# Optimization experiments

Hardware: AMD Instinct MI355X
Metric: run time of the kernel (lower is better)

The kernel has to match this reference:

```python
import jax, jax.numpy as jnp
import numpy as np

B, N, H, HEADS, PH, VD = 32, 256, 768, 12, 128, 16
DH = H // HEADS
VOCAB = 2 * VD + 3


def layer_norm(x, g, b, eps=1e-5):
    m = jnp.mean(x, axis=-1, keepdims=True)
    v = jnp.mean((x - m) ** 2, axis=-1, keepdims=True)
    return (x - m) * jax.lax.rsqrt(v + eps) * g + b


def setup_inputs() -> dict:
    key = jax.random.key(0)
    ks = jax.random.split(key, 12)
    # clamped relative-distance index pool, as in PathEmbeddingDistance
    t = np.arange(N)
    pool = t[None, :] - t[:, None]
    pool = np.clip(pool, -VD - 1, VD + 1) + VD + 1  # in [0, 2*VD+2]
    s = 0.02
    return {
        "nodes": jax.random.normal(ks[0], (B, N, H), jnp.float32),
        "bias": jnp.zeros((B, 1, 1, N), jnp.float32),
        "path_pool": jnp.asarray(pool, jnp.int32),
        "pos_table": jax.random.normal(ks[1], (VOCAB, PH), jnp.float32) * s,
        "Wq": jax.random.normal(ks[2], (H, H), jnp.float32) * s, "bq": jnp.zeros((H,), jnp.float32),
        "Wk": jax.random.normal(ks[3], (H, H), jnp.float32) * s, "bk": jnp.zeros((H,), jnp.float32),
        "Wv": jax.random.normal(ks[4], (H, H), jnp.float32) * s, "bv": jnp.zeros((H,), jnp.float32),
        "Wsk": jax.random.normal(ks[5], (PH, DH), jnp.float32) * s, "bsk": jnp.zeros((DH,), jnp.float32),
        "Wsv": jax.random.normal(ks[6], (PH, DH), jnp.float32) * s, "bsv": jnp.zeros((DH,), jnp.float32),
        "Wo": jax.random.normal(ks[7], (H, H), jnp.float32) * s, "bo": jnp.zeros((H,), jnp.float32),
        "g_path": jnp.ones((PH,), jnp.float32), "b_path": jnp.zeros((PH,), jnp.float32),
        "g_norm": jnp.ones((H,), jnp.float32), "b_norm": jnp.zeros((H,), jnp.float32),
    }


def reference(nodes, bias, path_pool, pos_table, Wq, bq, Wk, bk, Wv, bv,
              Wsk, bsk, Wsv, bsv, Wo, bo, g_path, b_path, g_norm, b_norm):
    # path embedding lookup (batch-independent: torch expand == broadcast)
    paths = pos_table[path_pool]                      # (N, N, PH)
    paths = layer_norm(paths, g_path, b_path)
    q = (nodes @ Wq + bq).reshape(B, N, HEADS, DH).transpose(0, 2, 1, 3)
    k = (nodes @ Wk + bk).reshape(B, N, HEADS, DH).transpose(0, 2, 1, 3)
    v = (nodes @ Wv + bv).reshape(B, N, HEADS, DH).transpose(0, 2, 1, 3)
    struct_k = paths @ Wsk + bsk                      # (N, N, DH)
    struct_v = paths @ Wsv + bsv                      # (N, N, DH)
    q = q * (DH ** -0.5)
    w = jnp.einsum("bhid,bhjd->bhij", q, k)
    struct_w = jnp.einsum("bhid,ijd->bhij", q, struct_k)
    w = jax.nn.softmax(w + struct_w + bias, axis=-1)  # (B, HEADS, N, N)
    out = jnp.einsum("bhij,bhjd->bhid", w, v) + jnp.einsum("bhij,ijd->bhid", w, struct_v)
    out = out.transpose(0, 2, 1, 3).reshape(B, N, H)  # combine heads
    out = jax.nn.relu(out @ Wo + bo)
    return layer_norm(nodes + out, g_norm, b_norm), w
```

## Files before the change

### kernel.cpp

```cpp
#include <hip/hip_runtime.h>
#include <hip/hip_bf16.h>

#define BB 32
#define NN 256
#define HH 768
#define NHEADS 12
#define DH 64
#define PHDIM 128
#define NVOCAB 35

typedef short bf16x8 __attribute__((ext_vector_type(8)));
typedef float f32x16 __attribute__((ext_vector_type(16)));
typedef unsigned u32x2 __attribute__((ext_vector_type(2)));

#define MFMA32 __builtin_amdgcn_mfma_f32_32x32x16_bf16

__device__ __forceinline__ unsigned short f2bf(float f) {
    unsigned u = __float_as_uint(f);
    unsigned r = (u + 0x7fffu + ((u >> 16) & 1u)) >> 16;
    return (unsigned short)r;
}

__device__ __forceinline__ unsigned pk2(float a, float b) {
    return (unsigned)f2bf(a) | ((unsigned)f2bf(b) << 16);
}

__device__ __forceinline__ bf16x8 pack8(const float f[8]) {
    bf16x8 r;
#pragma unroll
    for (int e = 0; e < 8; ++e) r[e] = (short)f2bf(f[e]);
    return r;
}

__global__ __launch_bounds__(256) void k_cast(const float* __restrict__ in,
                                              unsigned short* __restrict__ out) {
    int i = (blockIdx.x * 256 + threadIdx.x) * 4;
    float4 v = *reinterpret_cast<const float4*>(&in[i]);
    ushort4 o;
    o.x = f2bf(v.x); o.y = f2bf(v.y); o.z = f2bf(v.z); o.w = f2bf(v.w);
    *reinterpret_cast<ushort4*>(&out[i]) = o;
}

__global__ __launch_bounds__(256) void k_prep_w(
        const float* __restrict__ Wq, const float* __restrict__ Wk,
        const float* __restrict__ Wv, const float* __restrict__ Wo,
        unsigned short* __restrict__ Wt) {
    __shared__ unsigned short tile[64][72];
    int z = blockIdx.z;
    const float* W = (z == 0) ? Wq : (z == 1) ? Wk : (z == 2) ? Wv : Wo;
    unsigned short* out = Wt + (size_t)z * HH * HH;
    int k0 = blockIdx.x * 64, c0 = blockIdx.y * 64;
    int tid = threadIdx.x;
#pragma unroll
    for (int l = 0; l < 16; ++l) {
        int e = tid + l * 256;
        int r = e >> 6, c = e & 63;
        tile[c][r] = f2bf(W[(size_t)(k0 + r) * HH + c0 + c]);
    }
    __syncthreads();
#pragma unroll
    for (int l = 0; l < 2; ++l) {
        int e = tid + l * 256;
        int c = e >> 3, ch = e & 7;
        *reinterpret_cast<bf16x8*>(&out[(size_t)(c0 + c) * HH + k0 + ch * 8]) =
            *reinterpret_cast<const bf16x8*>(&tile[c][ch * 8]);
    }
}

__global__ void k_vocab(const float* __restrict__ pos_table,
                        const float* __restrict__ g_path, const float* __restrict__ b_path,
                        const float* __restrict__ Wsk, const float* __restrict__ bsk,
                        const float* __restrict__ Wsv, const float* __restrict__ bsv,
                        unsigned short* __restrict__ skv_bf, unsigned short* __restrict__ svv_t_bf) {
    int v = blockIdx.x;
    int t = threadIdx.x;
    if (v >= NVOCAB) {
        if (t < 64) skv_bf[v * 64 + t] = 0;
        else if (v < 48) svv_t_bf[(t - 64) * 48 + v] = 0;
        return;
    }
    __shared__ float x[PHDIM];
    __shared__ float red[PHDIM];
    float xv = pos_table[v * PHDIM + t];
    red[t] = xv;
    __syncthreads();
    for (int s = 64; s > 0; s >>= 1) { if (t < s) red[t] += red[t + s]; __syncthreads(); }
    float mean = red[0] / PHDIM;
    __syncthreads();
    float c = xv - mean;
    red[t] = c * c;
    __syncthreads();
    for (int s = 64; s > 0; s >>= 1) { if (t < s) red[t] += red[t + s]; __syncthreads(); }
    float var = red[0] / PHDIM;
    float ln = (xv - mean) * rsqrtf(var + 1e-5f) * g_path[t] + b_path[t];
    __syncthreads();
    x[t] = ln;
    __syncthreads();
    if (t < 64) {
        float acc = bsk[t];
        for (int p = 0; p < PHDIM; ++p) acc += x[p] * Wsk[p * DH + t];
        skv_bf[v * 64 + t] = f2bf(acc);
    } else {
        int d = t - 64;
        float acc = bsv[d];
        for (int p = 0; p < PHDIM; ++p) acc += x[p] * Wsv[p * DH + d];
        svv_t_bf[d * 48 + v] = f2bf(acc);
    }
}

__global__ __launch_bounds__(256) void k_qkv(
        const unsigned short* __restrict__ Abf, const unsigned short* __restrict__ Wt,
        const float* __restrict__ bq, const float* __restrict__ bk, const float* __restrict__ bv,
        unsigned short* __restrict__ q_bf, unsigned short* __restrict__ k_bf,
        unsigned short* __restrict__ v_bf_t) {
    __shared__ unsigned short Al[2][128 * 32];
    __shared__ unsigned short Bl[2][128 * 32];
    __shared__ unsigned short vstage[128][136];

    const int tid = threadIdx.x;
    const int w = tid >> 6, lane = tid & 63;
    const int il = lane & 31, hi = lane >> 5;
    const int wr = w >> 1, wc = w & 1;
    const int rowBase = blockIdx.x * 128;
    const int colBase = blockIdx.y * 128;
    const int sel = colBase / HH;
    const int jjBase0 = colBase - sel * HH;
    const float* bias = (sel == 0) ? bq : (sel == 1) ? bk : bv;

    f32x16 acc[2][2] = {};

    auto STAGE = [&](int buf, int k0) {
#pragma unroll
        for (int c = 0; c < 2; ++c) {
            int e = tid + c * 256;
            int row = e >> 2;
            int cb = (e & 3) << 4;
            int sc = cb ^ (((row >> 1) & 3) << 4);
            __builtin_amdgcn_global_load_lds(
                (const __attribute__((address_space(1))) unsigned int*)(Abf + (size_t)(rowBase + row) * HH + k0 + (sc >> 1)),
                (__attribute__((address_space(3))) unsigned int*)(&Al[buf][row * 32 + (cb >> 1)]), 16, 0, 0);
            __builtin_amdgcn_global_load_lds(
                (const __attribute__((address_space(1))) unsigned int*)(Wt + (size_t)(colBase + row) * HH + k0 + (sc >> 1)),
                (__attribute__((address_space(3))) unsigned int*)(&Bl[buf][row * 32 + (cb >> 1)]), 16, 0, 0);
        }
    };

    STAGE(0, 0);
    __syncthreads();
    for (int t = 0; t < 24; ++t) {
        int buf = t & 1;
        if (t < 23) STAGE(buf ^ 1, (t + 1) * 32);
#pragma unroll
        for (int ks = 0; ks < 2; ++ks) {
            bf16x8 af[2], bfr[2];
            int cb = (ks << 5) + (hi << 4);
#pragma unroll
            for (int t2 = 0; t2 < 2; ++t2) {
                int rrow = wr * 64 + t2 * 32 + il;
                af[t2] = *reinterpret_cast<const bf16x8*>(
                    &Al[buf][rrow * 32 + ((cb ^ (((rrow >> 1) & 3) << 4)) >> 1)]);
                int crow = wc * 64 + t2 * 32 + il;
                bfr[t2] = *reinterpret_cast<const bf16x8*>(
                    &Bl[buf][crow * 32 + ((cb ^ (((crow >> 1) & 3) << 4)) >> 1)]);
            }
            acc[0][0] = MFMA32(af[0], bfr[0], acc[0][0], 0, 0, 0);
            acc[0][1] = MFMA32(af[0], bfr[1], acc[0][1], 0, 0, 0);
            acc[1][0] = MFMA32(af[1], bfr[0], acc[1][0], 0, 0, 0);
            acc[1][1] = MFMA32(af[1], bfr[1], acc[1][1], 0, 0, 0);
        }
        __syncthreads();
    }

    if (sel < 2) {
        unsigned short* outp = (sel == 0) ? q_bf : k_bf;
        float scale = (sel == 0) ? 0.125f : 1.0f;
#pragma unroll
        for (int rt = 0; rt < 2; ++rt)
#pragma unroll
            for (int ct = 0; ct < 2; ++ct) {
                int jjB = jjBase0 + wc * 64 + ct * 32;
                int h = jjB >> 6, d = (jjB & 63) + il;
                float bias_v = bias[jjB + il];
#pragma unroll
                for (int r = 0; r < 16; ++r) {
                    int row = rowBase + wr * 64 + rt * 32 + ((r & 3) + 8 * (r >> 2) + 4 * hi);
                    int b = row >> 8, n = row & 255;
                    outp[((size_t)(b * NHEADS + h) * NN + n) * DH + d] =
                        f2bf((acc[rt][ct][r] + bias_v) * scale);
                }
            }
    } else {
#pragma unroll
        for (int rt = 0; rt < 2; ++rt)
#pragma unroll
            for (int ct = 0; ct < 2; ++ct) {
                int jjB = jjBase0 + wc * 64 + ct * 32;
                float bias_v = bias[jjB + il];
#pragma unroll
                for (int r = 0; r < 16; ++r) {
                    int rl = wr * 64 + rt * 32 + ((r & 3) + 8 * (r >> 2) + 4 * hi);
                    vstage[wc * 64 + ct * 32 + il][rl] = f2bf(acc[rt][ct][r] + bias_v);
                }
            }
        __syncthreads();
        int b = rowBase >> 8, n0 = rowBase & 255;
        int h0 = jjBase0 >> 6;
#pragma unroll
        for (int l = 0; l < 8; ++l) {
            int e = tid + l * 256;
            int cl = e >> 4;
            int nch = e & 15;
            size_t orow = (size_t)(b * NHEADS + h0 + (cl >> 6)) * DH + (cl & 63);
            *reinterpret_cast<bf16x8*>(&v_bf_t[orow * NN + n0 + nch * 8]) =
                *reinterpret_cast<const bf16x8*>(&vstage[cl][nch * 8]);
        }
    }
}

__global__ __launch_bounds__(256, 4) void k_attn(
        const unsigned short* __restrict__ q_bf, const unsigned short* __restrict__ k_bf,
        const unsigned short* __restrict__ v_bf_t,
        const unsigned short* __restrict__ skv_bf, const unsigned short* __restrict__ svv_t_bf,
        const float* __restrict__ bias,
        float* __restrict__ wout, unsigned short* __restrict__ attn_out) {
    __shared__ __align__(16) float qs_s[32][36];
    __shared__ __align__(16) float wsum[32][48];
    __shared__ __align__(16) float oex[3][32][68];
    __shared__ float msum[4][32][2];
    __shared__ float bias_s[NN];

    const int bx0 = blockIdx.x;
    const int bx = (bx0 & 7) * 384 + (bx0 >> 3);
    const int bh = bx >> 3, rowblk = bx & 7;
    const int b = bh / NHEADS, h = bh - b * NHEADS;
    const int tid = threadIdx.x;
    const int w = tid >> 6, lane = tid & 63;
    const int il = lane & 31, hi = lane >> 5;
    const int i0 = rowblk * 32;
    const int ig = i0 + il;
    const int jb = w * 64;

    bias_s[tid] = bias[b * NN + tid];
#pragma unroll
    for (int z = 0; z < 6; ++z) ((float*)wsum)[tid + z * 256] = 0.f;

    bf16x8 qf[4];
#pragma unroll
    for (int kt = 0; kt < 4; ++kt)
        qf[kt] = *reinterpret_cast<const bf16x8*>(
            &q_bf[((size_t)(bh * NN + ig)) * 64 + kt * 16 + 8 * hi]);

    if (w == 0) {
        f32x16 qa0 = {}, qa1 = {};
#pragma unroll
        for (int kt = 0; kt < 4; ++kt) {
            bf16x8 s0 = *reinterpret_cast<const bf16x8*>(&skv_bf[(size_t)il * 64 + kt * 16 + 8 * hi]);
            bf16x8 s1 = *reinterpret_cast<const bf16x8*>(&skv_bf[(size_t)(32 + il) * 64 + kt * 16 + 8 * hi]);
            qa0 = MFMA32(qf[kt], s0, qa0, 0, 0, 0);
            qa1 = MFMA32(qf[kt], s1, qa1, 0, 0, 0);
        }
#pragma unroll
        for (int r = 0; r < 16; ++r) {
            int ir = (r & 3) + 8 * (r >> 2) + 4 * hi;
            qs_s[ir][il] = qa0[r];
            if (il < 3) qs_s[ir][32 + il] = qa1[r];
        }
    }

    f32x16 S[2] = {};
#pragma unroll
    for (int jt = 0; jt < 2; ++jt) {
#pragma unroll
        for (int kt = 0; kt < 4; ++kt) {
            bf16x8 kf = *reinterpret_cast<const bf16x8*>(
                &k_bf[((size_t)(bh * NN + jb + jt * 32 + il)) * 64 + kt * 16 + 8 * hi]);
            S[jt] = MFMA32(kf, qf[kt], S[jt], 0, 0, 0);
        }
    }

    __syncthreads();

    {
        float qlo = qs_s[il][0], qhi = qs_s[il][34];
#pragma unroll
        for (int jt = 0; jt < 2; ++jt) {
#pragma unroll
            for (int rg = 0; rg < 4; ++rg) {
                int j0 = jb + jt * 32 + rg * 8 + 4 * hi;
                float4 bv4 = *reinterpret_cast<const float4*>(&bias_s[j0]);
                float bvf[4] = {bv4.x, bv4.y, bv4.z, bv4.w};
#pragma unroll
                for (int e = 0; e < 4; ++e) {
                    int dd = j0 + e - ig;
                    float sw = (dd < -16) ? qlo : (dd > 16) ? qhi : qs_s[il][dd + 17];
                    S[jt][rg * 4 + e] += bvf[e] + sw;
                }
            }
        }
    }

    float m = -3.4e38f;
#pragma unroll
    for (int jt = 0; jt < 2; ++jt)
#pragma unroll
        for (int r = 0; r < 16; ++r) m = fmaxf(m, S[jt][r]);
    m = fmaxf(m, __shfl_xor(m, 32));
    float sum = 0.f;
#pragma unroll
    for (int jt = 0; jt < 2; ++jt)
#pragma unroll
        for (int r = 0; r < 16; ++r) { float p = __expf(S[jt][r] - m); S[jt][r] = p; sum += p; }
    sum += __shfl_xor(sum, 32);
    if (hi == 0) { msum[w][il][0] = m; msum[w][il][1] = sum; }
    __syncthreads();

    {
        float m0 = msum[0][il][0], m1 = msum[1][il][0];
        float m2 = msum[2][il][0], m3 = msum[3][il][0];
        float M = fmaxf(fmaxf(m0, m1), fmaxf(m2, m3));
        float sumT = msum[0][il][1] * __expf(m0 - M) + msum[1][il][1] * __expf(m1 - M) +
                     msum[2][il][1] * __expf(m2 - M) + msum[3][il][1] * __expf(m3 - M);
        float scale = __expf(m - M) / sumT;
#pragma unroll
        for (int jt = 0; jt < 2; ++jt)
#pragma unroll
            for (int r = 0; r < 16; ++r) S[jt][r] *= scale;
    }

#pragma unroll
    for (int jt = 0; jt < 2; ++jt) {
#pragma unroll
        for (int rg = 0; rg < 4; ++rg) {
            float4 val;
            val.x = S[jt][rg * 4 + 0];
            val.y = S[jt][rg * 4 + 1];
            val.z = S[jt][rg * 4 + 2];
            val.w = S[jt][rg * 4 + 3];
            *reinterpret_cast<float4*>(
                &wout[((size_t)(bh * NN + ig)) * NN + jb + jt * 32 + rg * 8 + 4 * hi]) = val;
        }
    }

    {
        float elo = 0.f, ehi = 0.f;
#pragma unroll
        for (int jt = 0; jt < 2; ++jt)
#pragma unroll
            for (int r = 0; r < 16; ++r) {
                int j = jb + jt * 32 + (r & 3) + 8 * (r >> 2) + 4 * hi;
                int dd = j - ig;
                float p = S[jt][r];
                if (dd < -16) elo += p;
                else if (dd > 16) ehi += p;
                else wsum[il][dd + 17] = p;
            }
        if (elo != 0.f) atomicAdd(&wsum[il][0], elo);
        if (ehi != 0.f) atomicAdd(&wsum[il][34], ehi);
    }

    const unsigned short* vrow0 = &v_bf_t[((size_t)bh * 64 + il) * NN];
    const unsigned short* vrow1 = &v_bf_t[((size_t)bh * 64 + 32 + il) * NN];
    f32x16 O0 = {}, O1 = {};
#pragma unroll
    for (int jt = 0; jt < 2; ++jt) {
#pragma unroll
        for (int ks = 0; ks < 2; ++ks) {
            unsigned w0 = pk2(S[jt][8 * ks + 0], S[jt][8 * ks + 1]);
            unsigned w1 = pk2(S[jt][8 * ks + 2], S[jt][8 * ks + 3]);
            unsigned w2 = pk2(S[jt][8 * ks + 4], S[jt][8 * ks + 5]);
            unsigned w3 = pk2(S[jt][8 * ks + 6], S[jt][8 * ks + 7]);
            unsigned s0 = hi ? w0 : w2, s1 = hi ? w1 : w3;
            unsigned y0 = (unsigned)__shfl_xor((int)s0, 32);
            unsigned y1 = (unsigned)__shfl_xor((int)s1, 32);
            union { bf16x8 v; unsigned u[4]; } Bf;
            Bf.u[0] = hi ? y0 : w0;
            Bf.u[1] = hi ? y1 : w1;
            Bf.u[2] = hi ? w2 : y0;
            Bf.u[3] = hi ? w3 : y1;
            bf16x8 va0 = *reinterpret_cast<const bf16x8*>(&vrow0[jb + jt * 32 + ks * 16 + 8 * hi]);
            bf16x8 va1 = *reinterpret_cast<const bf16x8*>(&vrow1[jb + jt * 32 + ks * 16 + 8 * hi]);
            O0 = MFMA32(va0, Bf.v, O0, 0, 0, 0);
            O1 = MFMA32(va1, Bf.v, O1, 0, 0, 0);
        }
    }

    if (w != 0) {
#pragma unroll
        for (int qq = 0; qq < 4; ++qq) {
            int d0 = 8 * qq + 4 * hi;
            *reinterpret_cast<float4*>(&oex[w - 1][il][d0]) =
                float4{O0[4 * qq + 0], O0[4 * qq + 1], O0[4 * qq + 2], O0[4 * qq + 3]};
            *reinterpret_cast<float4*>(&oex[w - 1][il][32 + d0]) =
                float4{O1[4 * qq + 0], O1[4 * qq + 1], O1[4 * qq + 2], O1[4 * qq + 3]};
        }
    }
    __syncthreads();

    if (w == 0) {
#pragma unroll
        for (int s = 0; s < 3; ++s) {
#pragma unroll
            for (int qq = 0; qq < 4; ++qq) {
                int d0 = 8 * qq + 4 * hi;
                float4 p0 = *reinterpret_cast<const float4*>(&oex[s][il][d0]);
                float4 p1 = *reinterpret_cast<const float4*>(&oex[s][il][32 + d0]);
                O0[4 * qq + 0] += p0.x; O0[4 * qq + 1] += p0.y;
                O0[4 * qq + 2] += p0.z; O0[4 * qq + 3] += p0.w;
                O1[4 * qq + 0] += p1.x; O1[4 * qq + 1] += p1.y;
                O1[4 * qq + 2] += p1.z; O1[4 * qq + 3] += p1.w;
            }
        }

#pragma unroll
        for (int kt = 0; kt < 3; ++kt) {
            float4 a0 = *reinterpret_cast<const float4*>(&wsum[il][kt * 16 + 8 * hi]);
            float4 a1 = *reinterpret_cast<const float4*>(&wsum[il][kt * 16 + 8 * hi + 4]);
            float af[8] = {a0.x, a0.y, a0.z, a0.w, a1.x, a1.y, a1.z, a1.w};
            bf16x8 Bf = pack8(af);
            bf16x8 sa0 = *reinterpret_cast<const bf16x8*>(&svv_t_bf[(size_t)il * 48 + kt * 16 + 8 * hi]);
            bf16x8 sa1 = *reinterpret_cast<const bf16x8*>(&svv_t_bf[(size_t)(32 + il) * 48 + kt * 16 + 8 * hi]);
            O0 = MFMA32(sa0, Bf, O0, 0, 0, 0);
            O1 = MFMA32(sa1, Bf, O1, 0, 0, 0);
        }

#pragma unroll
        for (int qq = 0; qq < 4; ++qq) {
            int d0 = 8 * qq + 4 * hi;
            u32x2 o0, o1;
            o0[0] = pk2(O0[4 * qq + 0], O0[4 * qq + 1]);
            o0[1] = pk2(O0[4 * qq + 2], O0[4 * qq + 3]);
            o1[0] = pk2(O1[4 * qq + 0], O1[4 * qq + 1]);
            o1[1] = pk2(O1[4 * qq + 2], O1[4 * qq + 3]);
            size_t base = ((size_t)(b * NN + i0 + il)) * HH + h * 64;
            *reinterpret_cast<u32x2*>(&attn_out[base + d0]) = o0;
            *reinterpret_cast<u32x2*>(&attn_out[base + 32 + d0]) = o1;
        }
    }
}

__global__ __launch_bounds__(256) void k_ogemm(
        const unsigned short* __restrict__ Abf, const unsigned short* __restrict__ Bt,
        const float* __restrict__ bo, unsigned short* __restrict__ Cout) {
    __shared__ unsigned short Al[2][128 * 32];
    __shared__ unsigned short Bl[2][128 * 32];

    const int tid = threadIdx.x;
    const int w = tid >> 6, lane = tid & 63;
    const int il = lane & 31, hi = lane >> 5;
    const int wr = w >> 1, wc = w & 1;
    const int rowBase = blockIdx.x * 128;
    const int colBase = blockIdx.y * 128;

    f32x16 acc[2][2] = {};

    auto STAGE = [&](int buf, int k0) {
#pragma unroll
        for (int c = 0; c < 2; ++c) {
            int e = tid + c * 256;
            int row = e >> 2;
            int cb = (e & 3) << 4;
            int sc = cb ^ (((row >> 1) & 3) << 4);
            __builtin_amdgcn_global_load_lds(
                (const __attribute__((address_space(1))) unsigned int*)(Abf + (size_t)(rowBase + row) * HH + k0 + (sc >> 1)),
                (__attribute__((address_space(3))) unsigned int*)(&Al[buf][row * 32 + (cb >> 1)]), 16, 0, 0);
            __builtin_amdgcn_global_load_lds(
                (const __attribute__((address_space(1))) unsigned int*)(Bt + (size_t)(colBase + row) * HH + k0 + (sc >> 1)),
                (__attribute__((address_space(3))) unsigned int*)(&Bl[buf][row * 32 + (cb >> 1)]), 16, 0, 0);
        }
    };

    STAGE(0, 0);
    __syncthreads();
    for (int t = 0; t < 24; ++t) {
        int buf = t & 1;
        if (t < 23) STAGE(buf ^ 1, (t + 1) * 32);
#pragma unroll
        for (int ks = 0; ks < 2; ++ks) {
            bf16x8 af[2], bfr[2];
            int cb = (ks << 5) + (hi << 4);
#pragma unroll
            for (int t2 = 0; t2 < 2; ++t2) {
                int rrow = wr * 64 + t2 * 32 + il;
                af[t2] = *reinterpret_cast<const bf16x8*>(
                    &Al[buf][rrow * 32 + ((cb ^ (((rrow >> 1) & 3) << 4)) >> 1)]);
                int crow = wc * 64 + t2 * 32 + il;
                bfr[t2] = *reinterpret_cast<const bf16x8*>(
                    &Bl[buf][crow * 32 + ((cb ^ (((crow >> 1) & 3) << 4)) >> 1)]);
            }
            acc[0][0] = MFMA32(af[0], bfr[0], acc[0][0], 0, 0, 0);
            acc[0][1] = MFMA32(af[0], bfr[1], acc[0][1], 0, 0, 0);
            acc[1][0] = MFMA32(af[1], bfr[0], acc[1][0], 0, 0, 0);
            acc[1][1] = MFMA32(af[1], bfr[1], acc[1][1], 0, 0, 0);
        }
        __syncthreads();
    }

#pragma unroll
    for (int rt = 0; rt < 2; ++rt)
#pragma unroll
        for (int ct = 0; ct < 2; ++ct) {
            int col = colBase + wc * 64 + ct * 32 + il;
            float bias_v = bo[col];
#pragma unroll
            for (int r = 0; r < 16; ++r) {
                int row = rowBase + wr * 64 + rt * 32 + ((r & 3) + 8 * (r >> 2) + 4 * hi);
                Cout[(size_t)row * HH + col] = f2bf(fmaxf(acc[rt][ct][r] + bias_v, 0.f));
            }
        }
}

__global__ __launch_bounds__(256) void k_ln(
        const float* __restrict__ nodes, const unsigned short* __restrict__ proj,
        const float* __restrict__ g, const float* __restrict__ bta,
        float* __restrict__ out) {
    __shared__ float red[2][4];
    int row = blockIdx.x;
    int tid = threadIdx.x;
    int w = tid >> 6, lane = tid & 63;
    float x[3];
    float s = 0.f, s2 = 0.f;
#pragma unroll
    for (int l = 0; l < 3; ++l) {
        int c = tid + l * 256;
        float pv = __uint_as_float(((unsigned)proj[(size_t)row * HH + c]) << 16);
        x[l] = nodes[(size_t)row * HH + c] + pv;
        s += x[l];
        s2 += x[l] * x[l];
    }
#pragma unroll
    for (int off = 32; off > 0; off >>= 1) {
        s += __shfl_xor(s, off);
        s2 += __shfl_xor(s2, off);
    }
    if (lane == 0) { red[0][w] = s; red[1][w] = s2; }
    __syncthreads();
    float ts = red[0][0] + red[0][1] + red[0][2] + red[0][3];
    float ts2 = red[1][0] + red[1][1] + red[1][2] + red[1][3];
    float mean = ts / HH;
    float var = ts2 / HH - mean * mean;
    float inv = rsqrtf(fmaxf(var, 0.f) + 1e-5f);
#pragma unroll
    for (int l = 0; l < 3; ++l) {
        int c = tid + l * 256;
        out[(size_t)row * HH + c] = (x[l] - mean) * inv * g[c] + bta[c];
    }
}

extern "C" void kernel_launch(void* const* d_in, const int* in_sizes, int n_in,
                              void* d_out, int out_size, void* d_ws, size_t ws_size,
                              hipStream_t stream) {
    const float* nodes     = (const float*)d_in[0];
    const float* bias      = (const float*)d_in[1];
    const float* pos_table = (const float*)d_in[3];
    const float* Wq = (const float*)d_in[4];  const float* bq = (const float*)d_in[5];
    const float* Wk = (const float*)d_in[6];  const float* bk = (const float*)d_in[7];
    const float* Wv = (const float*)d_in[8];  const float* bv = (const float*)d_in[9];
    const float* Wsk = (const float*)d_in[10]; const float* bsk = (const float*)d_in[11];
    const float* Wsv = (const float*)d_in[12]; const float* bsv = (const float*)d_in[13];
    const float* Wo = (const float*)d_in[14]; const float* bo = (const float*)d_in[15];
    const float* g_path = (const float*)d_in[16]; const float* b_path = (const float*)d_in[17];
    const float* g_norm = (const float*)d_in[18]; const float* b_norm = (const float*)d_in[19];

    float* out0 = (float*)d_out;
    float* wout = out0 + (size_t)BB * NN * HH;

    const size_t per = (size_t)BB * NN * HH;
    char* p = (char*)d_ws;
    unsigned short* q_bf    = (unsigned short*)p; p += per * 2;
    unsigned short* k_bf    = (unsigned short*)p; p += per * 2;
    unsigned short* v_bf_t  = (unsigned short*)p; p += per * 2;
    unsigned short* skv_bf  = (unsigned short*)p; p += 64 * 64 * 2;
    unsigned short* svv_t   = (unsigned short*)p; p += 64 * 48 * 2;
    unsigned short* nodes_bf= (unsigned short*)p; p += per * 2;
    unsigned short* Wt      = (unsigned short*)p; p += (size_t)4 * HH * HH * 2;
    unsigned short* attn_bf = (unsigned short*)p; p += per * 2;
    unsigned short* proj_bf = v_bf_t;

    k_cast<<<per / 4 / 256, 256, 0, stream>>>(nodes, nodes_bf);

    dim3 gw(12, 12, 4);
    k_prep_w<<<gw, 256, 0, stream>>>(Wq, Wk, Wv, Wo, Wt);

    k_vocab<<<64, 128, 0, stream>>>(pos_table, g_path, b_path, Wsk, bsk, Wsv, bsv, skv_bf, svv_t);

    dim3 g2(64, 18);
    k_qkv<<<g2, 256, 0, stream>>>(nodes_bf, Wt, bq, bk, bv, q_bf, k_bf, v_bf_t);

    k_attn<<<BB * NHEADS * 8, 256, 0, stream>>>(q_bf, k_bf, v_bf_t, skv_bf, svv_t, bias, wout, attn_bf);

    dim3 g4(64, 6);
    k_ogemm<<<g4, 256, 0, stream>>>(attn_bf, Wt + (size_t)3 * HH * HH, bo, proj_bf);

    k_ln<<<BB * NN, 256, 0, stream>>>(nodes, proj_bf, g_norm, b_norm, out0);
}
```

Measured before the change: 158.4 us.

## Store Q/K/V in MFMA fragment order and merge prep kernels into one launch

```diff
diff --git a/kernel.cpp b/kernel.cpp
--- a/kernel.cpp
+++ b/kernel.cpp
@@ -32,79 +32,86 @@
     return r;
 }
 
-__global__ __launch_bounds__(256) void k_cast(const float* __restrict__ in,
-                                              unsigned short* __restrict__ out) {
-    int i = (blockIdx.x * 256 + threadIdx.x) * 4;
-    float4 v = *reinterpret_cast<const float4*>(&in[i]);
-    ushort4 o;
-    o.x = f2bf(v.x); o.y = f2bf(v.y); o.z = f2bf(v.z); o.w = f2bf(v.w);
-    *reinterpret_cast<ushort4*>(&out[i]) = o;
-}
-
-__global__ __launch_bounds__(256) void k_prep_w(
+__global__ __launch_bounds__(256) void k_prep(
+        const float* __restrict__ nodes, unsigned short* __restrict__ nodes_bf,
         const float* __restrict__ Wq, const float* __restrict__ Wk,
         const float* __restrict__ Wv, const float* __restrict__ Wo,
-        unsigned short* __restrict__ Wt) {
-    __shared__ unsigned short tile[64][72];
-    int z = blockIdx.z;
-    const float* W = (z == 0) ? Wq : (z == 1) ? Wk : (z == 2) ? Wv : Wo;
-    unsigned short* out = Wt + (size_t)z * HH * HH;
-    int k0 = blockIdx.x * 64, c0 = blockIdx.y * 64;
-    int tid = threadIdx.x;
-#pragma unroll
-    for (int l = 0; l < 16; ++l) {
-        int e = tid + l * 256;
-        int r = e >> 6, c = e & 63;
-        tile[c][r] = f2bf(W[(size_t)(k0 + r) * HH + c0 + c]);
-    }
-    __syncthreads();
-#pragma unroll
-    for (int l = 0; l < 2; ++l) {
-        int e = tid + l * 256;
-        int c = e >> 3, ch = e & 7;
-        *reinterpret_cast<bf16x8*>(&out[(size_t)(c0 + c) * HH + k0 + ch * 8]) =
-            *reinterpret_cast<const bf16x8*>(&tile[c][ch * 8]);
-    }
-}
-
-__global__ void k_vocab(const float* __restrict__ pos_table,
-                        const float* __restrict__ g_path, const float* __restrict__ b_path,
-                        const float* __restrict__ Wsk, const float* __restrict__ bsk,
-                        const float* __restrict__ Wsv, const float* __restrict__ bsv,
-                        unsigned short* __restrict__ skv_bf, unsigned short* __restrict__ svv_t_bf) {
-    int v = blockIdx.x;
-    int t = threadIdx.x;
-    if (v >= NVOCAB) {
-        if (t < 64) skv_bf[v * 64 + t] = 0;
-        else if (v < 48) svv_t_bf[(t - 64) * 48 + v] = 0;
+        unsigned short* __restrict__ Wt,
+        const float* __restrict__ pos_table,
+        const float* __restrict__ g_path, const float* __restrict__ b_path,
+        const float* __restrict__ Wsk, const float* __restrict__ bsk,
+        const float* __restrict__ Wsv, const float* __restrict__ bsv,
+        unsigned short* __restrict__ skv_bf, unsigned short* __restrict__ svv_t_bf) {
+    const int blk = blockIdx.x;
+    const int tid = threadIdx.x;
+
+    if (blk < 6144) {
+        int i = (blk * 256 + tid) * 4;
+        float4 v = *reinterpret_cast<const float4*>(&nodes[i]);
+        ushort4 o;
+        o.x = f2bf(v.x); o.y = f2bf(v.y); o.z = f2bf(v.z); o.w = f2bf(v.w);
+        *reinterpret_cast<ushort4*>(&nodes_bf[i]) = o;
         return;
     }
-    __shared__ float x[PHDIM];
-    __shared__ float red[PHDIM];
-    float xv = pos_table[v * PHDIM + t];
-    red[t] = xv;
-    __syncthreads();
-    for (int s = 64; s > 0; s >>= 1) { if (t < s) red[t] += red[t + s]; __syncthreads(); }
-    float mean = red[0] / PHDIM;
-    __syncthreads();
-    float c = xv - mean;
-    red[t] = c * c;
-    __syncthreads();
-    for (int s = 64; s > 0; s >>= 1) { if (t < s) red[t] += red[t + s]; __syncthreads(); }
-    float var = red[0] / PHDIM;
-    float ln = (xv - mean) * rsqrtf(var + 1e-5f) * g_path[t] + b_path[t];
-    __syncthreads();
-    x[t] = ln;
-    __syncthreads();
-    if (t < 64) {
-        float acc = bsk[t];
-        for (int p = 0; p < PHDIM; ++p) acc += x[p] * Wsk[p * DH + t];
-        skv_bf[v * 64 + t] = f2bf(acc);
-    } else {
-        int d = t - 64;
-        float acc = bsv[d];
-        for (int p = 0; p < PHDIM; ++p) acc += x[p] * Wsv[p * DH + d];
-        svv_t_bf[d * 48 + v] = f2bf(acc);
+
+    if (blk < 6720) {
+        __shared__ unsigned short tile[64][72];
+        int wb = blk - 6144;
+        int z = wb / 144;
+        int rem = wb - z * 144;
+        int k0 = (rem / 12) * 64, c0 = (rem % 12) * 64;
+        const float* W = (z == 0) ? Wq : (z == 1) ? Wk : (z == 2) ? Wv : Wo;
+        unsigned short* out = Wt + (size_t)z * HH * HH;
+#pragma unroll
+        for (int l = 0; l < 16; ++l) {
+            int e = tid + l * 256;
+            int r = e >> 6, c = e & 63;
+            tile[c][r] = f2bf(W[(size_t)(k0 + r) * HH + c0 + c]);
+        }
+        __syncthreads();
+#pragma unroll
+        for (int l = 0; l < 2; ++l) {
+            int e = tid + l * 256;
+            int c = e >> 3, ch = e & 7;
+            *reinterpret_cast<bf16x8*>(&out[(size_t)(c0 + c) * HH + k0 + ch * 8]) =
+                *reinterpret_cast<const bf16x8*>(&tile[c][ch * 8]);
+        }
+        return;
+    }
+
+    {
+        int v = blk - 6720;
+        int t = tid;
+        if (v >= NVOCAB) {
+            if (t < 64) skv_bf[v * 64 + t] = 0;
+            else if (t < 128 && v < 48) svv_t_bf[(t - 64) * 48 + v] = 0;
+            return;
+        }
+        __shared__ float x[PHDIM];
+        __shared__ float red[PHDIM];
+        float xv = 0.f;
+        if (t < PHDIM) { xv = pos_table[v * PHDIM + t]; red[t] = xv; }
+        __syncthreads();
+        for (int s = 64; s > 0; s >>= 1) { if (t < s) red[t] += red[t + s]; __syncthreads(); }
+        float mean = red[0] / PHDIM;
+        __syncthreads();
+        if (t < PHDIM) { float c = xv - mean; red[t] = c * c; }
+        __syncthreads();
+        for (int s = 64; s > 0; s >>= 1) { if (t < s) red[t] += red[t + s]; __syncthreads(); }
+        float var = red[0] / PHDIM;
+        __syncthreads();
+        if (t < PHDIM) x[t] = (xv - mean) * rsqrtf(var + 1e-5f) * g_path[t] + b_path[t];
+        __syncthreads();
+        if (t < 64) {
+            float acc = bsk[t];
+            for (int p = 0; p < PHDIM; ++p) acc += x[p] * Wsk[p * DH + t];
+            skv_bf[v * 64 + t] = f2bf(acc);
+        } else if (t < 128) {
+            int d = t - 64;
+            float acc = bsv[d];
+            for (int p = 0; p < PHDIM; ++p) acc += x[p] * Wsv[p * DH + d];
+            svv_t_bf[d * 48 + v] = f2bf(acc);
+        }
     }
 }
 
@@ -179,14 +186,18 @@
 #pragma unroll
             for (int ct = 0; ct < 2; ++ct) {
                 int jjB = jjBase0 + wc * 64 + ct * 32;
-                int h = jjB >> 6, d = (jjB & 63) + il;
+                int h = jjB >> 6;
+                int d = ct * 32 + il;
+                int kt = d >> 4, hif = (d >> 3) & 1, e = d & 7;
                 float bias_v = bias[jjB + il];
 #pragma unroll
                 for (int r = 0; r < 16; ++r) {
                     int row = rowBase + wr * 64 + rt * 32 + ((r & 3) + 8 * (r >> 2) + 4 * hi);
                     int b = row >> 8, n = row & 255;
-                    outp[((size_t)(b * NHEADS + h) * NN + n) * DH + d] =
-                        f2bf((acc[rt][ct][r] + bias_v) * scale);
+                    int jr = n & 31, t32 = n >> 5;
+                    size_t off = ((((size_t)(b * NHEADS + h) * 8 + t32) * 4 + kt) * 64 +
+                                  (hif * 32 + jr)) * 8 + e;
+                    outp[off] = f2bf((acc[rt][ct][r] + bias_v) * scale);
                 }
             }
     } else {
@@ -207,12 +218,20 @@
         int h0 = jjBase0 >> 6;
 #pragma unroll
         for (int l = 0; l < 8; ++l) {
-            int e = tid + l * 256;
-            int cl = e >> 4;
-            int nch = e & 15;
-            size_t orow = (size_t)(b * NHEADS + h0 + (cl >> 6)) * DH + (cl & 63);
-            *reinterpret_cast<bf16x8*>(&v_bf_t[orow * NN + n0 + nch * 8]) =
-                *reinterpret_cast<const bf16x8*>(&vstage[cl][nch * 8]);
+            int idx = tid + l * 256;
+            int cl = idx >> 4;
+            int ch = idx & 15;
+            int tl0 = ch * 8;
+            int dg = cl & 63;
+            int bh = b * NHEADS + h0 + (cl >> 6);
+            int tok0 = n0 + tl0;
+            int jt = tok0 >> 5, rem = tok0 & 31;
+            int ks = rem >> 4, hif = (rem >> 3) & 1;
+            int dh = dg >> 5;
+            int lanef = hif * 32 + (dg & 31);
+            size_t off = (((((size_t)bh * 8 + jt) * 2 + ks) * 2 + dh) * 64 + lanef) * 8;
+            *reinterpret_cast<bf16x8*>(&v_bf_t[off]) =
+                *reinterpret_cast<const bf16x8*>(&vstage[cl][tl0]);
         }
     }
 }
@@ -238,7 +257,6 @@
     const int il = lane & 31, hi = lane >> 5;
     const int i0 = rowblk * 32;
     const int ig = i0 + il;
-    const int jb = w * 64;
 
     bias_s[tid] = bias[b * NN + tid];
 #pragma unroll
@@ -248,7 +266,7 @@
 #pragma unroll
     for (int kt = 0; kt < 4; ++kt)
         qf[kt] = *reinterpret_cast<const bf16x8*>(
-            &q_bf[((size_t)(bh * NN + ig)) * 64 + kt * 16 + 8 * hi]);
+            &q_bf[((((size_t)bh * 8 + rowblk) * 4 + kt) * 64 + lane) * 8]);
 
     if (w == 0) {
         f32x16 qa0 = {}, qa1 = {};
@@ -270,16 +288,18 @@
     f32x16 S[2] = {};
 #pragma unroll
     for (int jt = 0; jt < 2; ++jt) {
+        int jtg = w * 2 + jt;
 #pragma unroll
         for (int kt = 0; kt < 4; ++kt) {
             bf16x8 kf = *reinterpret_cast<const bf16x8*>(
-                &k_bf[((size_t)(bh * NN + jb + jt * 32 + il)) * 64 + kt * 16 + 8 * hi]);
+                &k_bf[((((size_t)bh * 8 + jtg) * 4 + kt) * 64 + lane) * 8]);
             S[jt] = MFMA32(kf, qf[kt], S[jt], 0, 0, 0);
         }
     }
 
     __syncthreads();
 
+    const int jb = w * 64;
     {
         float qlo = qs_s[il][0], qhi = qs_s[il][34];
 #pragma unroll
@@ -358,11 +378,10 @@
         if (ehi != 0.f) atomicAdd(&wsum[il][34], ehi);
     }
 
-    const unsigned short* vrow0 = &v_bf_t[((size_t)bh * 64 + il) * NN];
-    const unsigned short* vrow1 = &v_bf_t[((size_t)bh * 64 + 32 + il) * NN];
     f32x16 O0 = {}, O1 = {};
 #pragma unroll
     for (int jt = 0; jt < 2; ++jt) {
+        int jtg = w * 2 + jt;
 #pragma unroll
         for (int ks = 0; ks < 2; ++ks) {
             unsigned w0 = pk2(S[jt][8 * ks + 0], S[jt][8 * ks + 1]);
@@ -377,8 +396,10 @@
             Bf.u[1] = hi ? y1 : w1;
             Bf.u[2] = hi ? w2 : y0;
             Bf.u[3] = hi ? w3 : y1;
-            bf16x8 va0 = *reinterpret_cast<const bf16x8*>(&vrow0[jb + jt * 32 + ks * 16 + 8 * hi]);
-            bf16x8 va1 = *reinterpret_cast<const bf16x8*>(&vrow1[jb + jt * 32 + ks * 16 + 8 * hi]);
+            bf16x8 va0 = *reinterpret_cast<const bf16x8*>(
+                &v_bf_t[(((((size_t)bh * 8 + jtg) * 2 + ks) * 2 + 0) * 64 + lane) * 8]);
+            bf16x8 va1 = *reinterpret_cast<const bf16x8*>(
+                &v_bf_t[(((((size_t)bh * 8 + jtg) * 2 + ks) * 2 + 1) * 64 + lane) * 8]);
             O0 = MFMA32(va0, Bf.v, O0, 0, 0, 0);
             O1 = MFMA32(va1, Bf.v, O1, 0, 0, 0);
         }
@@ -576,12 +597,9 @@
     unsigned short* attn_bf = (unsigned short*)p; p += per * 2;
     unsigned short* proj_bf = v_bf_t;
 
-    k_cast<<<per / 4 / 256, 256, 0, stream>>>(nodes, nodes_bf);
-
-    dim3 gw(12, 12, 4);
-    k_prep_w<<<gw, 256, 0, stream>>>(Wq, Wk, Wv, Wo, Wt);
-
-    k_vocab<<<64, 128, 0, stream>>>(pos_table, g_path, b_path, Wsk, bsk, Wsv, bsv, skv_bf, svv_t);
+    k_prep<<<6784, 256, 0, stream>>>(nodes, nodes_bf, Wq, Wk, Wv, Wo, Wt,
+                                     pos_table, g_path, b_path, Wsk, bsk, Wsv, bsv,
+                                     skv_bf, svv_t);
 
     dim3 g2(64, 18);
     k_qkv<<<g2, 256, 0, stream>>>(nodes_bf, Wt, bq, bk, bv, q_bf, k_bf, v_bf_t);
```

Result: faster. 149.1 us (-5.8%).
